# Kernel tuning notes

Measured on AMD Instinct MI355X. Metric: run time of the kernel, lower is better.

## Reference

```python
import jax, jax.numpy as jnp
import numpy as np
import math

B, S, D, H = 32, 197, 1024, 16  # batch, seq_len (pinned by w_o=Linear(197,.)), d_model, n_heads
DK = D // H                      # d_k = 64


def setup_inputs() -> dict:
    key = jax.random.key(0)
    ks = jax.random.split(key, 8)
    f32 = jnp.float32
    # weights scaled by 0.02 for numerically sane softmax logits
    return {
        "x0": jax.random.normal(ks[0], (B, S, D), dtype=f32),
        "x1": jax.random.normal(ks[1], (B, S, D), dtype=f32),
        "wk0": jax.random.normal(ks[2], (D, D), dtype=f32) * 0.02,
        "bk0": jnp.zeros((D,), dtype=f32),
        "wk1": jax.random.normal(ks[3], (D, D), dtype=f32) * 0.02,
        "bk1": jnp.zeros((D,), dtype=f32),
        "wv0": jax.random.normal(ks[4], (D, D), dtype=f32) * 0.02,
        "bv0": jnp.zeros((D,), dtype=f32),
        "wv1": jax.random.normal(ks[5], (D, D), dtype=f32) * 0.02,
        "bv1": jnp.zeros((D,), dtype=f32),
        "wo": jax.random.normal(ks[6], (D, S), dtype=f32) * 0.02,  # nn.Linear(197, d_model) weight: [d_model, 197]
        "bo": jnp.zeros((D,), dtype=f32),
    }


def _proj(x, w, b):
    # torch nn.Linear: y = x @ W^T + b; then view + transpose -> [B, H, S, DK]
    y = x @ w.T + b
    return y.reshape(B, S, H, DK).transpose(0, 2, 1, 3)


def reference(x0, x1, wk0, bk0, wk1, bk1, wv0, bv0, wv1, bv1, wo, bo):
    scale = 1.0 / math.sqrt(DK)
    K0 = _proj(x0, wk0, bk0)
    K1 = _proj(x1, wk1, bk1)
    V0 = _proj(x0, wv0, bv0)
    V1 = _proj(x1, wv1, bv1)
    # mutual attention: K_i @ K_j^T * scale for i != j  -> [B, H, S, S]
    s01 = jnp.einsum('bhsd,bhtd->bhst', K0, K1) * scale
    s10 = jnp.einsum('bhsd,bhtd->bhst', K1, K0) * scale
    a0 = jax.nn.softmax(s01, axis=-1)
    a1 = jax.nn.softmax(s10, axis=-1)
    # feature outputs: attn_i @ V_i  -> [B, H, S, DK]
    f0 = jnp.einsum('bhst,bhtd->bhsd', a0, V0)
    f1 = jnp.einsum('bhst,bhtd->bhsd', a1, V1)
    # cross-product combination, averaged over the 2 ordered pairs -> [B, H, S, S]
    comb = (jnp.einsum('bhsd,bhtd->bhst', f0, f1)
            + jnp.einsum('bhsd,bhtd->bhst', f1, f0)) * (scale * 0.5)
    # w_o: Linear(197 -> d_model) on last axis -> [B, H, S, D]
    out = comb @ wo.T + bo
    return (out, a0, a1)
```

## Files before the change

kernel.cpp:

```cpp
#include <hip/hip_runtime.h>
#include <hip/hip_bf16.h>

typedef unsigned short u16;
typedef __attribute__((ext_vector_type(8))) short short8;
typedef __attribute__((ext_vector_type(4))) float floatx4;
typedef __attribute__((ext_vector_type(4), aligned(4))) float floatx4u;
typedef __attribute__((ext_vector_type(4))) unsigned int uint4v;

#define B_ 32
#define S_ 197
#define D_ 1024
#define H_ 16
#define DK_ 64
#define BH_ 512
#define SP_ 208
#define TP_ 224
#define TPP_ 232
#define M_ 6304
#define XSZ_ ((size_t)M_*D_)
#define WSZ_W ((size_t)D_*D_)

#define KSZ ((size_t)BH_*SP_*DK_)
#define VSZ ((size_t)BH_*DK_*TP_)
#define CSZ ((size_t)BH_*SP_*TP_)
#define K0_OFF  ((size_t)0)
#define K1_OFF  (KSZ)
#define VT0_OFF (2*KSZ)
#define VT1_OFF (2*KSZ + VSZ)
#define F0_OFF  (2*KSZ + 2*VSZ)
#define F1_OFF  (3*KSZ + 2*VSZ)
#define COMB_OFF (4*KSZ + 2*VSZ)
#define WOT_OFF  (4*KSZ + 2*VSZ + CSZ)
#define BIAS_OFF (WOT_OFF + (size_t)D_*TP_)
#define WS_ELEMS (BIAS_OFF + 5*1024)

#define XB_OFF  (COMB_OFF)
#define WB_OFF  (COMB_OFF + 2*XSZ_)

#define OUT_SZ ((size_t)BH_*S_*D_)
#define A_SZ   ((size_t)BH_*S_*S_)

__device__ __forceinline__ float bf2f(u16 v) {
    unsigned u = ((unsigned)v) << 16;
    return __builtin_bit_cast(float, u);
}
__device__ __forceinline__ u16 f2bf(float f) {
    unsigned u = __builtin_bit_cast(unsigned, f);
    u += 0x7FFFu + ((u >> 16) & 1u);
    return (u16)(u >> 16);
}
__device__ __forceinline__ floatx4 mfma16(short8 a, short8 b, floatx4 c) {
    return __builtin_amdgcn_mfma_f32_16x16x32_bf16(a, b, c, 0, 0, 0);
}
__device__ __forceinline__ void gl_lds16(const u16* g, u16* l) {
    __builtin_amdgcn_global_load_lds(
        (const __attribute__((address_space(1))) void*)(g),
        (__attribute__((address_space(3))) void*)(l), 16, 0, 0);
}

__device__ __forceinline__ int detect_f32(const u16* __restrict__ x0raw) {
    int lane = threadIdx.x & 63;
    unsigned h = x0raw[2*lane];
    unsigned e = (h >> 7) & 0xFFu;
    int ext = (e < 0x30u) | (e > 0x4Fu);
    unsigned long long m = __ballot(ext);
    return __popcll(m) > 16;
}

__device__ __forceinline__ u16 loadBF(const void* p, size_t off, int is32) {
    return is32 ? f2bf(((const float*)p)[off]) : ((const u16*)p)[off];
}
__device__ __forceinline__ void storeF(void* p, size_t off, float v, int is32) {
    if (is32) ((float*)p)[off] = v; else ((u16*)p)[off] = f2bf(v);
}
__device__ __forceinline__ short8 load8(const void* p, size_t off, int is32) {
    short8 r;
    if (is32) {
        const float* f = (const float*)p + off;
        floatx4 a = *(const floatx4*)f;
        floatx4 b = *(const floatx4*)(f + 4);
        r[0]=(short)f2bf(a[0]); r[1]=(short)f2bf(a[1]);
        r[2]=(short)f2bf(a[2]); r[3]=(short)f2bf(a[3]);
        r[4]=(short)f2bf(b[0]); r[5]=(short)f2bf(b[1]);
        r[6]=(short)f2bf(b[2]); r[7]=(short)f2bf(b[3]);
    } else {
        r = *(const short8*)((const u16*)p + off);
    }
    return r;
}

__global__ __launch_bounds__(256) void prep_kernel(
    const void* __restrict__ wo,
    const void* __restrict__ bk0, const void* __restrict__ bk1,
    const void* __restrict__ bv0, const void* __restrict__ bv1,
    const void* __restrict__ bo,
    const void* __restrict__ x0, const void* __restrict__ x1,
    const void* __restrict__ wk0, const void* __restrict__ wk1,
    const void* __restrict__ wv0, const void* __restrict__ wv1,
    u16* __restrict__ ws) {
    int is32 = detect_f32((const u16*)x0);
    int i = blockIdx.x * 256 + threadIdx.x;
    if (i < D_*TP_) {
        int d = i / TP_, t = i - d*TP_;
        ws[WOT_OFF + i] = (t < S_) ? loadBF(wo, (size_t)d*S_ + t, is32) : (u16)0;
    }
    const int KP = BH_*(SP_-S_)*DK_;
    if (i < KP) {
        int bh = i / ((SP_-S_)*DK_);
        int r  = i - bh*((SP_-S_)*DK_);
        int s  = S_ + r / DK_;
        int dk = r % DK_;
        size_t o = ((size_t)bh*SP_ + s)*DK_ + dk;
        ws[K0_OFF + o] = 0; ws[K1_OFF + o] = 0;
    }
    const int VP = BH_*DK_*(TP_-S_);
    if (i < VP) {
        int bh = i / (DK_*(TP_-S_));
        int r  = i - bh*(DK_*(TP_-S_));
        int dk = r / (TP_-S_);
        int t  = S_ + r % (TP_-S_);
        size_t o = ((size_t)bh*DK_ + dk)*TP_ + t;
        ws[VT0_OFF + o] = 0; ws[VT1_OFF + o] = 0;
    }
    if (i < 5*1024) {
        int which = i >> 10, j = i & 1023;
        const void* src = (which==0) ? bk0 : (which==1) ? bk1
                        : (which==2) ? bv0 : (which==3) ? bv1 : bo;
        ws[BIAS_OFF + i] = loadBF(src, j, is32);
    }
    const size_t NCH = (2*XSZ_ + 4*WSZ_W) / 8;
    for (size_t c = (size_t)blockIdx.x*256 + threadIdx.x; c < NCH;
         c += (size_t)gridDim.x*256) {
        size_t e = c * 8;
        const void* src; size_t soff;
        if (e < 2*XSZ_) {
            src = (e < XSZ_) ? x0 : x1;
            soff = (e < XSZ_) ? e : e - XSZ_;
        } else {
            size_t r = e - 2*XSZ_;
            int z = (int)(r >> 20);
            src = (z==0) ? wk0 : (z==1) ? wk1 : (z==2) ? wv0 : wv1;
            soff = r & (WSZ_W - 1);
        }
        *(short8*)&ws[XB_OFF + e] = load8(src, soff, is32);
    }
}

__global__ __launch_bounds__(256) void proj_kernel(u16* __restrict__ ws)
{
    __shared__ __align__(16) u16 lA[128*64];
    __shared__ __align__(16) u16 lB[128*64];
    int L = blockIdx.x;
    int o = (L & 7) * 200 + (L >> 3);
    int bx = o % 50;
    int yz = o / 50;
    int by = yz & 7;
    int z  = yz >> 3;
    const u16* X = ws + XB_OFF + (size_t)(z & 1)*XSZ_;
    const u16* W = ws + WB_OFF + (size_t)z*WSZ_W;
    u16* dst = ws + ((z==0) ? K0_OFF : (z==1) ? K1_OFF : (z==2) ? VT0_OFF : VT1_OFF);
    int m0 = bx * 128, n0 = by * 128;
    int tid = threadIdx.x;
    int w = tid >> 6, lane = tid & 63, q = lane >> 4, l15 = lane & 15;
    int wm = (w >> 1) * 64, wn = (w & 1) * 64;

    floatx4 acc[4][4];
    #pragma unroll
    for (int a = 0; a < 4; a++)
        #pragma unroll
        for (int b = 0; b < 4; b++) acc[a][b] = (floatx4){0.f,0.f,0.f,0.f};

    for (int kk = 0; kk < D_; kk += 64) {
        __syncthreads();
        #pragma unroll
        for (int it = 0; it < 4; it++) {
            int c = it*256 + w*64 + lane;
            int r = c >> 3, cc = c & 7;
            int m = m0 + r; if (m > M_-1) m = M_-1;
            gl_lds16(X + (size_t)m*D_ + kk + cc*8,        &lA[(it*256 + w*64)*8]);
            gl_lds16(W + (size_t)(n0 + r)*D_ + kk + cc*8, &lB[(it*256 + w*64)*8]);
        }
        __syncthreads();
        #pragma unroll
        for (int kc = 0; kc < 2; kc++) {
            short8 af[4], bf[4];
            #pragma unroll
            for (int mi = 0; mi < 4; mi++)
                af[mi] = *(const short8*)&lA[(wm + mi*16 + l15)*64 + kc*32 + q*8];
            #pragma unroll
            for (int ni = 0; ni < 4; ni++)
                bf[ni] = *(const short8*)&lB[(wn + ni*16 + l15)*64 + kc*32 + q*8];
            #pragma unroll
            for (int mi = 0; mi < 4; mi++)
                #pragma unroll
                for (int ni = 0; ni < 4; ni++)
                    acc[mi][ni] = mfma16(af[mi], bf[ni], acc[mi][ni]);
        }
    }
    #pragma unroll
    for (int ni = 0; ni < 4; ni++) {
        int n = n0 + wn + ni*16 + l15;
        float bv = bf2f(ws[BIAS_OFF + (size_t)z*1024 + n]);
        int h = n >> 6, dk = n & 63;
        #pragma unroll
        for (int mi = 0; mi < 4; mi++)
            #pragma unroll
            for (int r = 0; r < 4; r++) {
                int m = m0 + wm + mi*16 + q*4 + r;
                if (m < M_) {
                    int b = m / S_;
                    int s = m - b * S_;
                    int bh = b * H_ + h;
                    size_t o2 = (z < 2) ? (((size_t)bh*SP_ + s)*DK_ + dk)
                                        : (((size_t)bh*DK_ + dk)*TP_ + s);
                    dst[o2] = f2bf(acc[mi][ni][r] + bv);
                }
            }
    }
}

__global__ __launch_bounds__(256) void attn_av_kernel(u16* __restrict__ ws,
                                                      void* __restrict__ dout,
                                                      const u16* __restrict__ x0det) {
    __shared__ __align__(16) u16 lKb[SP_*DK_];
    __shared__ __align__(16) u16 lP[4][16*TPP_];
    int is32 = detect_f32(x0det);
    int bh = blockIdx.x, dir = blockIdx.y;
    const u16* Ka = ws + (dir ? K1_OFF : K0_OFF) + (size_t)bh*SP_*DK_;
    const u16* Kb = ws + (dir ? K0_OFF : K1_OFF) + (size_t)bh*SP_*DK_;
    const u16* Vt = ws + (dir ? VT1_OFF : VT0_OFF) + (size_t)bh*DK_*TP_;
    u16* fO = ws + (dir ? F1_OFF : F0_OFF) + (size_t)bh*SP_*DK_;
    size_t aBase = OUT_SZ + (size_t)dir*A_SZ + (size_t)bh*S_*S_;
    int tid = threadIdx.x;
    for (int i = tid; i < SP_*8; i += 256)
        ((uint4v*)lKb)[(i & ~7) | ((i ^ (i >> 3)) & 7)] = ((const uint4v*)Kb)[i];
    __syncthreads();
    int w = tid>>6, lane = tid&63, q = lane>>4, l15 = lane&15;
    u16* lPw = &lP[w][0];
    const float scale = 0.125f;
    for (int rt = w; rt < 13; rt += 4) {
        floatx4 acc[13];
        #pragma unroll
        for (int ct = 0; ct < 13; ct++) acc[ct] = (floatx4){0.f,0.f,0.f,0.f};
        #pragma unroll
        for (int kc = 0; kc < 2; kc++) {
            short8 af = *(const short8*)&Ka[(size_t)(rt*16 + l15)*DK_ + kc*32 + q*8];
            #pragma unroll
            for (int ct = 0; ct < 13; ct++) {
                short8 bf = *(const short8*)&lKb[(ct*16 + l15)*DK_ +
                                                 ((kc*32 + q*8) ^ ((l15 & 7) << 3))];
                acc[ct] = mfma16(af, bf, acc[ct]);
            }
        }
        #pragma unroll
        for (int r = 0; r < 4; r++) {
            int srow = rt*16 + q*4 + r;
            float v[13];
            float mx = -1e9f;
            #pragma unroll
            for (int ct = 0; ct < 13; ct++) {
                int t = ct*16 + l15;
                v[ct] = (t < S_) ? acc[ct][r]*scale : -1e9f;
                mx = fmaxf(mx, v[ct]);
            }
            #pragma unroll
            for (int off = 1; off < 16; off <<= 1) mx = fmaxf(mx, __shfl_xor(mx, off));
            float sum = 0.f;
            #pragma unroll
            for (int ct = 0; ct < 13; ct++) {
                int t = ct*16 + l15;
                float e = (t < S_) ? __expf(v[ct] - mx) : 0.f;
                v[ct] = e; sum += e;
            }
            #pragma unroll
            for (int off = 1; off < 16; off <<= 1) sum += __shfl_xor(sum, off);
            float inv = 1.0f / sum;
            bool rok = srow < S_;
            #pragma unroll
            for (int ct = 0; ct < 13; ct++) {
                int t = ct*16 + l15;
                float pv = rok ? v[ct]*inv : 0.f;
                lPw[(q*4 + r)*TPP_ + ct*16 + l15] = f2bf(pv);
                if (rok && t < S_) storeF(dout, aBase + (size_t)srow*S_ + t, pv, is32);
            }
            lPw[(q*4 + r)*TPP_ + 208 + l15] = 0;
        }
        floatx4 facc[4];
        #pragma unroll
        for (int ct = 0; ct < 4; ct++) facc[ct] = (floatx4){0.f,0.f,0.f,0.f};
        for (int kc = 0; kc < 7; kc++) {
            short8 paf = *(const short8*)&lPw[l15*TPP_ + kc*32 + q*8];
            #pragma unroll
            for (int ct = 0; ct < 4; ct++) {
                short8 bf = *(const short8*)&Vt[(size_t)(ct*16 + l15)*TP_ + kc*32 + q*8];
                facc[ct] = mfma16(paf, bf, facc[ct]);
            }
        }
        #pragma unroll
        for (int ct = 0; ct < 4; ct++)
            #pragma unroll
            for (int r = 0; r < 4; r++) {
                int so = rt*16 + q*4 + r;
                fO[(size_t)so*DK_ + ct*16 + l15] = f2bf(facc[ct][r]);
            }
    }
}

__global__ __launch_bounds__(512) void comb_out_kernel(const u16* __restrict__ ws,
                                                       void* __restrict__ dout,
                                                       const u16* __restrict__ x0det) {
    __shared__ __align__(16) u16 smem[SP_*TPP_ + 128*TPP_];
    u16* lC  = smem;
    u16* lw  = smem + SP_*TPP_;
    u16* lf0 = lw;
    u16* lf1 = lw + SP_*DK_;
    int is32 = detect_f32(x0det);
    int bh = blockIdx.x;
    const u16* f0 = ws + F0_OFF + (size_t)bh*SP_*DK_;
    const u16* f1 = ws + F1_OFF + (size_t)bh*SP_*DK_;
    size_t oBase = (size_t)bh*S_*D_;
    int tid = threadIdx.x;
    for (int i = tid; i < SP_*8; i += 512) {
        int d = (i & ~7) | ((i ^ (i >> 3)) & 7);
        ((uint4v*)lf0)[d] = ((const uint4v*)f0)[i];
        ((uint4v*)lf1)[d] = ((const uint4v*)f1)[i];
    }
    __syncthreads();
    int w = tid>>6, lane = tid&63, q = lane>>4, l15 = lane&15;
    int sw = (l15 & 7) << 3;
    const float cscale = 0.0625f;
    for (int rt = w; rt < 13; rt += 8) {
        short8 a0f[2], a1f[2];
        #pragma unroll
        for (int kc = 0; kc < 2; kc++) {
            int eo = (kc*32 + q*8) ^ sw;
            a0f[kc] = *(const short8*)&lf0[(rt*16 + l15)*DK_ + eo];
            a1f[kc] = *(const short8*)&lf1[(rt*16 + l15)*DK_ + eo];
        }
        for (int nt = 0; nt < 13; nt++) {
            floatx4 acc = (floatx4){0.f,0.f,0.f,0.f};
            #pragma unroll
            for (int kc = 0; kc < 2; kc++) {
                short8 b1 = *(const short8*)&lf1[(nt*16 + l15)*DK_ + ((kc*32 + q*8) ^ sw)];
                acc = mfma16(a0f[kc], b1, acc);
            }
            #pragma unroll
            for (int kc = 0; kc < 2; kc++) {
                short8 b0 = *(const short8*)&lf0[(nt*16 + l15)*DK_ + ((kc*32 + q*8) ^ sw)];
                acc = mfma16(a1f[kc], b0, acc);
            }
            #pragma unroll
            for (int r = 0; r < 4; r++) {
                int srow = rt*16 + q*4 + r;
                lC[srow*TPP_ + nt*16 + l15] = f2bf(acc[r]*cscale);
            }
        }
        #pragma unroll
        for (int r = 0; r < 4; r++) {
            int srow = rt*16 + q*4 + r;
            lC[srow*TPP_ + 208 + l15] = 0;
        }
    }
    __syncthreads();
    for (int nb = 0; nb < 8; nb++) {
        const u16* wot = ws + WOT_OFF + (size_t)nb*128*TP_;
        for (int i = tid; i < 128*28; i += 512) {
            int row = i / 28, c = i - row*28;
            ((uint4v*)lw)[row*29 + c] = ((const uint4v*)wot)[i];
        }
        __syncthreads();
        for (int mt = w; mt < 13; mt += 8) {
            floatx4 acc[8];
            #pragma unroll
            for (int nt = 0; nt < 8; nt++) acc[nt] = (floatx4){0.f,0.f,0.f,0.f};
            for (int kc = 0; kc < 7; kc++) {
                short8 af = *(const short8*)&lC[(mt*16 + l15)*TPP_ + kc*32 + q*8];
                #pragma unroll
                for (int nt = 0; nt < 8; nt++) {
                    short8 bf = *(const short8*)&lw[(nt*16 + l15)*TPP_ + kc*32 + q*8];
                    acc[nt] = mfma16(af, bf, acc[nt]);
                }
            }
            #pragma unroll
            for (int nt = 0; nt < 8; nt++) {
                int d = nb*128 + nt*16 + l15;
                float bv = bf2f(ws[BIAS_OFF + 4*1024 + d]);
                #pragma unroll
                for (int r = 0; r < 4; r++) {
                    int s = mt*16 + q*4 + r;
                    if (s < S_) storeF(dout, oBase + (size_t)s*D_ + d, acc[nt][r] + bv, is32);
                }
            }
        }
        __syncthreads();
    }
}

extern "C" void kernel_launch(void* const* d_in, const int* in_sizes, int n_in,
                              void* d_out, int out_size, void* d_ws, size_t ws_size,
                              hipStream_t stream) {
    const void* x0  = d_in[0];
    const void* x1  = d_in[1];
    const void* wk0 = d_in[2];
    const void* bk0 = d_in[3];
    const void* wk1 = d_in[4];
    const void* bk1 = d_in[5];
    const void* wv0 = d_in[6];
    const void* bv0 = d_in[7];
    const void* wv1 = d_in[8];
    const void* bv1 = d_in[9];
    const void* wo  = d_in[10];
    const void* bo  = d_in[11];
    u16* ws = (u16*)d_ws;
    const u16* x0det = (const u16*)x0;

    if (ws_size < WS_ELEMS * sizeof(u16)) return;

    prep_kernel<<<3456, 256, 0, stream>>>(wo, bk0, bk1, bv0, bv1, bo,
                                          x0, x1, wk0, wk1, wv0, wv1, ws);
    proj_kernel<<<1600, 256, 0, stream>>>(ws);
    attn_av_kernel<<<dim3(BH_, 2), 256, 0, stream>>>(ws, d_out, x0det);
    comb_out_kernel<<<BH_, 512, 0, stream>>>(ws, d_out, x0det);
}
```

Before: 1.071 ms.

## Split comb/out kernel via global comb buffer and drop LDS staging of K in attention

Splits the fused combination+output-projection kernel into a comb kernel that writes the combined scores to a global workspace buffer and an out kernel gridded over (bh, 64-column chunk). This removes the large per-block LDS footprint that limited occupancy and serialized the 8 output chunks per block. The attention kernel also reads the K operand directly from global/cache instead of staging it in LDS, and adds occupancy hints. The cost is an extra global round-trip for the comb matrix, repeated reads of it across 16 column blocks, and possibly less efficient uncoalesced K loads.

Measured after the change: 1.320 ms. 1.23x slower.

```diff
diff --git a/kernel.cpp b/kernel.cpp
--- a/kernel.cpp
+++ b/kernel.cpp
@@ -4,7 +4,6 @@
 typedef unsigned short u16;
 typedef __attribute__((ext_vector_type(8))) short short8;
 typedef __attribute__((ext_vector_type(4))) float floatx4;
-typedef __attribute__((ext_vector_type(4), aligned(4))) float floatx4u;
 typedef __attribute__((ext_vector_type(4))) unsigned int uint4v;
 
 #define B_ 32
@@ -219,10 +218,9 @@
     }
 }
 
-__global__ __launch_bounds__(256) void attn_av_kernel(u16* __restrict__ ws,
-                                                      void* __restrict__ dout,
-                                                      const u16* __restrict__ x0det) {
-    __shared__ __align__(16) u16 lKb[SP_*DK_];
+__global__ __launch_bounds__(256, 4) void attn_av_kernel(u16* __restrict__ ws,
+                                                         void* __restrict__ dout,
+                                                         const u16* __restrict__ x0det) {
     __shared__ __align__(16) u16 lP[4][16*TPP_];
     int is32 = detect_f32(x0det);
     int bh = blockIdx.x, dir = blockIdx.y;
@@ -232,9 +230,6 @@
     u16* fO = ws + (dir ? F1_OFF : F0_OFF) + (size_t)bh*SP_*DK_;
     size_t aBase = OUT_SZ + (size_t)dir*A_SZ + (size_t)bh*S_*S_;
     int tid = threadIdx.x;
-    for (int i = tid; i < SP_*8; i += 256)
-        ((uint4v*)lKb)[(i & ~7) | ((i ^ (i >> 3)) & 7)] = ((const uint4v*)Kb)[i];
-    __syncthreads();
     int w = tid>>6, lane = tid&63, q = lane>>4, l15 = lane&15;
     u16* lPw = &lP[w][0];
     const float scale = 0.125f;
@@ -247,8 +242,7 @@
             short8 af = *(const short8*)&Ka[(size_t)(rt*16 + l15)*DK_ + kc*32 + q*8];
             #pragma unroll
             for (int ct = 0; ct < 13; ct++) {
-                short8 bf = *(const short8*)&lKb[(ct*16 + l15)*DK_ +
-                                                 ((kc*32 + q*8) ^ ((l15 & 7) << 3))];
+                short8 bf = *(const short8*)&Kb[(size_t)(ct*16 + l15)*DK_ + kc*32 + q*8];
                 acc[ct] = mfma16(af, bf, acc[ct]);
             }
         }
@@ -306,93 +300,86 @@
     }
 }
 
-__global__ __launch_bounds__(512) void comb_out_kernel(const u16* __restrict__ ws,
-                                                       void* __restrict__ dout,
-                                                       const u16* __restrict__ x0det) {
-    __shared__ __align__(16) u16 smem[SP_*TPP_ + 128*TPP_];
-    u16* lC  = smem;
-    u16* lw  = smem + SP_*TPP_;
-    u16* lf0 = lw;
-    u16* lf1 = lw + SP_*DK_;
-    int is32 = detect_f32(x0det);
+__global__ __launch_bounds__(256, 8) void comb_kernel(u16* __restrict__ ws) {
     int bh = blockIdx.x;
     const u16* f0 = ws + F0_OFF + (size_t)bh*SP_*DK_;
     const u16* f1 = ws + F1_OFF + (size_t)bh*SP_*DK_;
+    u16* cO = ws + COMB_OFF + (size_t)bh*SP_*TP_;
+    int tid = threadIdx.x;
+    int w = tid>>6, lane = tid&63, q = lane>>4, l15 = lane&15;
+    const float cscale = 0.0625f;
+    for (int rt = w; rt < 13; rt += 4) {
+        short8 a0f[2], a1f[2];
+        #pragma unroll
+        for (int kc = 0; kc < 2; kc++) {
+            size_t eo = (size_t)(rt*16 + l15)*DK_ + kc*32 + q*8;
+            a0f[kc] = *(const short8*)&f0[eo];
+            a1f[kc] = *(const short8*)&f1[eo];
+        }
+        for (int nt = 0; nt < 13; nt++) {
+            floatx4 acc = (floatx4){0.f,0.f,0.f,0.f};
+            #pragma unroll
+            for (int kc = 0; kc < 2; kc++) {
+                short8 b1 = *(const short8*)&f1[(size_t)(nt*16 + l15)*DK_ + kc*32 + q*8];
+                acc = mfma16(a0f[kc], b1, acc);
+            }
+            #pragma unroll
+            for (int kc = 0; kc < 2; kc++) {
+                short8 b0 = *(const short8*)&f0[(size_t)(nt*16 + l15)*DK_ + kc*32 + q*8];
+                acc = mfma16(a1f[kc], b0, acc);
+            }
+            #pragma unroll
+            for (int r = 0; r < 4; r++) {
+                int srow = rt*16 + q*4 + r;
+                cO[(size_t)srow*TP_ + nt*16 + l15] = f2bf(acc[r]*cscale);
+            }
+        }
+        #pragma unroll
+        for (int r = 0; r < 4; r++) {
+            int srow = rt*16 + q*4 + r;
+            cO[(size_t)srow*TP_ + 208 + l15] = 0;
+        }
+    }
+}
+
+__global__ __launch_bounds__(256, 5) void out_kernel(const u16* __restrict__ ws,
+                                                     void* __restrict__ dout,
+                                                     const u16* __restrict__ x0det) {
+    __shared__ __align__(16) u16 lw[64*TPP_];
+    int is32 = detect_f32(x0det);
+    int bh = blockIdx.x, nb = blockIdx.y;
+    const u16* wot = ws + WOT_OFF + (size_t)nb*64*TP_;
+    const u16* cI  = ws + COMB_OFF + (size_t)bh*SP_*TP_;
     size_t oBase = (size_t)bh*S_*D_;
     int tid = threadIdx.x;
-    for (int i = tid; i < SP_*8; i += 512) {
-        int d = (i & ~7) | ((i ^ (i >> 3)) & 7);
-        ((uint4v*)lf0)[d] = ((const uint4v*)f0)[i];
-        ((uint4v*)lf1)[d] = ((const uint4v*)f1)[i];
+    for (int i = tid; i < 64*28; i += 256) {
+        int row = i / 28, c = i - row*28;
+        ((uint4v*)lw)[row*29 + c] = ((const uint4v*)wot)[i];
     }
     __syncthreads();
     int w = tid>>6, lane = tid&63, q = lane>>4, l15 = lane&15;
-    int sw = (l15 & 7) << 3;
-    const float cscale = 0.0625f;
-    for (int rt = w; rt < 13; rt += 8) {
-        short8 a0f[2], a1f[2];
-        #pragma unroll
-        for (int kc = 0; kc < 2; kc++) {
-            int eo = (kc*32 + q*8) ^ sw;
-            a0f[kc] = *(const short8*)&lf0[(rt*16 + l15)*DK_ + eo];
-            a1f[kc] = *(const short8*)&lf1[(rt*16 + l15)*DK_ + eo];
-        }
-        for (int nt = 0; nt < 13; nt++) {
-            floatx4 acc = (floatx4){0.f,0.f,0.f,0.f};
-            #pragma unroll
-            for (int kc = 0; kc < 2; kc++) {
-                short8 b1 = *(const short8*)&lf1[(nt*16 + l15)*DK_ + ((kc*32 + q*8) ^ sw)];
-                acc = mfma16(a0f[kc], b1, acc);
-            }
-            #pragma unroll
-            for (int kc = 0; kc < 2; kc++) {
-                short8 b0 = *(const short8*)&lf0[(nt*16 + l15)*DK_ + ((kc*32 + q*8) ^ sw)];
-                acc = mfma16(a1f[kc], b0, acc);
-            }
+    for (int mt = w; mt < 13; mt += 4) {
+        floatx4 acc[4];
+        #pragma unroll
+        for (int nt = 0; nt < 4; nt++) acc[nt] = (floatx4){0.f,0.f,0.f,0.f};
+        for (int kc = 0; kc < 7; kc++) {
+            short8 af = *(const short8*)&cI[(size_t)(mt*16 + l15)*TP_ + kc*32 + q*8];
+            #pragma unroll
+            for (int nt = 0; nt < 4; nt++) {
+                short8 bf = *(const short8*)&lw[(nt*16 + l15)*TPP_ + kc*32 + q*8];
+                acc[nt] = mfma16(af, bf, acc[nt]);
+            }
+        }
+        #pragma unroll
+        for (int nt = 0; nt < 4; nt++) {
+            int d = nb*64 + nt*16 + l15;
+            float bv = bf2f(ws[BIAS_OFF + 4*1024 + d]);
             #pragma unroll
             for (int r = 0; r < 4; r++) {
-                int srow = rt*16 + q*4 + r;
-                lC[srow*TPP_ + nt*16 + l15] = f2bf(acc[r]*cscale);
-            }
-        }
-        #pragma unroll
-        for (int r = 0; r < 4; r++) {
-            int srow = rt*16 + q*4 + r;
-            lC[srow*TPP_ + 208 + l15] = 0;
-        }
-    }
-    __syncthreads();
-    for (int nb = 0; nb < 8; nb++) {
-        const u16* wot = ws + WOT_OFF + (size_t)nb*128*TP_;
-        for (int i = tid; i < 128*28; i += 512) {
-            int row = i / 28, c = i - row*28;
-            ((uint4v*)lw)[row*29 + c] = ((const uint4v*)wot)[i];
-        }
-        __syncthreads();
-        for (int mt = w; mt < 13; mt += 8) {
-            floatx4 acc[8];
-            #pragma unroll
-            for (int nt = 0; nt < 8; nt++) acc[nt] = (floatx4){0.f,0.f,0.f,0.f};
-            for (int kc = 0; kc < 7; kc++) {
-                short8 af = *(const short8*)&lC[(mt*16 + l15)*TPP_ + kc*32 + q*8];
-                #pragma unroll
-                for (int nt = 0; nt < 8; nt++) {
-                    short8 bf = *(const short8*)&lw[(nt*16 + l15)*TPP_ + kc*32 + q*8];
-                    acc[nt] = mfma16(af, bf, acc[nt]);
-                }
-            }
-            #pragma unroll
-            for (int nt = 0; nt < 8; nt++) {
-                int d = nb*128 + nt*16 + l15;
-                float bv = bf2f(ws[BIAS_OFF + 4*1024 + d]);
-                #pragma unroll
-                for (int r = 0; r < 4; r++) {
-                    int s = mt*16 + q*4 + r;
-                    if (s < S_) storeF(dout, oBase + (size_t)s*D_ + d, acc[nt][r] + bv, is32);
-                }
-            }
-        }
-        __syncthreads();
+                int s = mt*16 + q*4 + r;
+                if (s < S_) storeF(dout, oBase + (size_t)s*D_ + d, acc[nt][r] + bv, is32);
+            }
+        }
     }
 }
 
@@ -420,5 +407,6 @@
                                           x0, x1, wk0, wk1, wv0, wv1, ws);
     proj_kernel<<<1600, 256, 0, stream>>>(ws);
     attn_av_kernel<<<dim3(BH_, 2), 256, 0, stream>>>(ws, d_out, x0det);
-    comb_out_kernel<<<BH_, 512, 0, stream>>>(ws, d_out, x0det);
-}
+    comb_kernel<<<BH_, 256, 0, stream>>>(ws);
+    out_kernel<<<dim3(BH_, 16), 256, 0, stream>>>(ws, d_out, x0det);
+}
```
